# Kernel tuning notes

Measured on AMD Instinct MI355X. Metric: run time of the kernel, lower is better.

Reference implementation:

```python
import jax, jax.numpy as jnp
import numpy as np

N, T, D, H = 256, 128, 512, 1024


def setup_inputs() -> dict:
    key = jax.random.key(0)
    k_x, k_A, k_Wx, k_Wh, k_Wa = jax.random.split(key, 5)
    x = jax.random.normal(k_x, (N, T, D), dtype=jnp.float32)
    A = jax.random.normal(k_A, (N, H, 4, 4), dtype=jnp.float32)
    Wx = jax.random.normal(k_Wx, (D, 4 * H), dtype=jnp.float32) / np.sqrt(D)
    Wh = jax.random.normal(k_Wh, (H, 4 * H), dtype=jnp.float32) / np.sqrt(H)
    Wattn = jax.random.normal(k_Wa, (H, 4 * H), dtype=jnp.float32) / np.sqrt(H)
    b = jnp.zeros((4 * H,), dtype=jnp.float32)
    return {"x": x, "A": A, "Wx": Wx, "Wh": Wh, "Wattn": Wattn, "b": b}


def _attention_lstm(x, A, Wx, Wh, Wattn, b):
    # A: (N, H, 4, 4) -> flatten spatial to (N, H, 16)
    A_flat = A.reshape(A.shape[0], A.shape[1], -1)
    h0 = A_flat.mean(axis=2)  # (N, H)
    c0 = h0
    Hdim = h0.shape[1]
    scale = 1.0 / jnp.sqrt(jnp.asarray(Hdim, dtype=x.dtype))

    def step(carry, x_t):
        prev_h, prev_c = carry
        # scaled dot-product attention over 16 spatial locations
        scores = jnp.einsum("nh,nhs->ns", prev_h, A_flat) * scale  # (N, 16)
        w = jax.nn.softmax(scores, axis=1)
        attn = jnp.einsum("nhs,ns->nh", A_flat, w)  # (N, H)
        # fused LSTM gates
        a = x_t @ Wx + prev_h @ Wh + attn @ Wattn + b  # (N, 4H)
        i = jax.nn.sigmoid(a[:, 0:Hdim])
        f = jax.nn.sigmoid(a[:, Hdim:2 * Hdim])
        o = jax.nn.sigmoid(a[:, 2 * Hdim:3 * Hdim])
        g = jnp.tanh(a[:, 3 * Hdim:4 * Hdim])
        next_c = f * prev_c + i * g
        next_h = o * jnp.tanh(next_c)
        return (next_h, next_c), next_h

    x_tnd = jnp.swapaxes(x, 0, 1)  # (T, N, D)
    _, h_tnh = jax.lax.scan(step, (h0, c0), x_tnd)
    return jnp.swapaxes(h_tnh, 0, 1)  # (N, T, H)


def reference(x, A, Wx, Wh, Wattn, b):
    return _attention_lstm(x, A, Wx, Wh, Wattn, b)
```

## Files before the change

### kernel.cpp

```cpp
#include <hip/hip_runtime.h>
#include <math.h>

#define NB 256
#define TT 128
#define DD 512
#define HH 1024
#define KHX 1536
#define KFB 2560
#define BK 128
#define NBLK3 256
#define NCH3 16

typedef _Float16 half_t;
typedef _Float16 half8 __attribute__((ext_vector_type(8)));
typedef _Float16 half4v __attribute__((ext_vector_type(4)));
typedef _Float16 half2v __attribute__((ext_vector_type(2)));
typedef float f32x4 __attribute__((ext_vector_type(4)));


__global__ __launch_bounds__(256) void k_trans(const float* __restrict__ src,
        half_t* __restrict__ dst, int kstride, int koff, int nkt) {
    __shared__ half_t tile[64][65];
    int bk = blockIdx.x % nkt;
    int bn = blockIdx.x / nkt;
    int k0 = bk * 64, n0 = bn * 64;
    #pragma unroll
    for (int i = 0; i < 16; ++i) {
        int idx = i * 256 + threadIdx.x;
        int r = idx >> 6, c = idx & 63;
        tile[c][r] = (half_t)src[(size_t)(k0 + r) * 4096 + n0 + c];
    }
    __syncthreads();
    #pragma unroll
    for (int i = 0; i < 16; ++i) {
        int idx = i * 256 + threadIdx.x;
        int r = idx >> 6, c = idx & 63;
        dst[(size_t)(n0 + r) * kstride + koff + k0 + c] = tile[r][c];
    }
}

__global__ __launch_bounds__(256) void k_convX(const float* __restrict__ x,
        half_t* __restrict__ x16) {
    size_t base = ((size_t)blockIdx.x * 256 + threadIdx.x) * 32;
    #pragma unroll
    for (int u = 0; u < 4; ++u) {
        float4 a = ((const float4*)(x + base))[2 * u];
        float4 c = ((const float4*)(x + base))[2 * u + 1];
        half8 p;
        p[0] = (half_t)a.x; p[1] = (half_t)a.y; p[2] = (half_t)a.z; p[3] = (half_t)a.w;
        p[4] = (half_t)c.x; p[5] = (half_t)c.y; p[6] = (half_t)c.z; p[7] = (half_t)c.w;
        ((half8*)(x16 + base))[u] = p;
    }
}

__global__ __launch_bounds__(256) void k_convA(const float* __restrict__ A,
        half_t* __restrict__ A16, half_t* __restrict__ AsT,
        float* __restrict__ cbuf, half_t* __restrict__ h16,
        float* __restrict__ sc0, float* __restrict__ sc1, float* __restrict__ sc2) {
    __shared__ float sred[4][16];
    int n = blockIdx.x, tid = threadIdx.x;
    float ps[16];
    #pragma unroll
    for (int s = 0; s < 16; ++s) ps[s] = 0.f;
    #pragma unroll
    for (int r = 0; r < 4; ++r) {
        int h = tid + r * 256;
        const float4* ap = (const float4*)(A + ((size_t)n * HH + h) * 16);
        float4 v0 = ap[0], v1 = ap[1], v2 = ap[2], v3 = ap[3];
        float a[16];
        a[0]=v0.x; a[1]=v0.y; a[2] =v0.z; a[3] =v0.w;
        a[4]=v1.x; a[5]=v1.y; a[6] =v1.z; a[7] =v1.w;
        a[8]=v2.x; a[9]=v2.y; a[10]=v2.z; a[11]=v2.w;
        a[12]=v3.x; a[13]=v3.y; a[14]=v3.z; a[15]=v3.w;
        float hv = 0.f;
        #pragma unroll
        for (int s = 0; s < 16; ++s) hv += a[s];
        hv *= (1.f / 16.f);
        size_t ci = (size_t)n * HH + h;
        cbuf[ci] = hv;
        h16[ci] = (half_t)hv;
        half8 q0, q1;
        #pragma unroll
        for (int s = 0; s < 8; ++s) { q0[s] = (half_t)a[s]; q1[s] = (half_t)a[s + 8]; }
        *(half8*)(A16 + ci * 16) = q0;
        *(half8*)(A16 + ci * 16 + 8) = q1;
        #pragma unroll
        for (int s = 0; s < 16; ++s)
            AsT[(size_t)n * 16 * HH + (size_t)s * HH + h] = (half_t)a[s];
        #pragma unroll
        for (int s = 0; s < 16; ++s) ps[s] += hv * a[s];
    }
    #pragma unroll
    for (int off = 32; off; off >>= 1)
        #pragma unroll
        for (int s = 0; s < 16; ++s) ps[s] += __shfl_xor(ps[s], off, 64);
    int wave = tid >> 6;
    if ((tid & 63) == 0)
        #pragma unroll
        for (int s = 0; s < 16; ++s) sred[wave][s] = ps[s];
    __syncthreads();
    if (tid < 16) {
        sc0[n * 16 + tid] = sred[0][tid] + sred[1][tid] + sred[2][tid] + sred[3][tid];
        sc1[n * 16 + tid] = 0.f;
        sc2[n * 16 + tid] = 0.f;
    }
}

__global__ __launch_bounds__(256) void k_gemm_G(const half_t* __restrict__ AsT,
        const half_t* __restrict__ WaT, half_t* __restrict__ G16) {
    __shared__ half_t sAs[16][BK + 8];
    __shared__ half_t sB[4][16][BK + 8];
    int bid = blockIdx.x;
    int n = bid >> 6, jt = bid & 63;
    int j0 = jt * 16;
    int tid = threadIdx.x, wv = tid >> 6, lane = tid & 63;
    f32x4 acc = {};
    int srB = tid >> 2, scB = (tid & 3) * 32;
    int gB = srB >> 4, jcB = srB & 15;
    for (int it = 0; it < HH / BK; ++it) {
        int k0 = it * BK;
        if (tid < 128) {
            int r = tid >> 3, c = (tid & 7) * 16;
            const uint4* sp = (const uint4*)(AsT + (size_t)n * 16 * HH + (size_t)r * HH + k0 + c);
            uint4 u0 = sp[0], u1 = sp[1];
            *(uint4*)&sAs[r][c] = u0;
            *(uint4*)&sAs[r][c + 8] = u1;
        }
        {
            const half_t* src = WaT + ((size_t)(gB * HH + j0 + jcB)) * HH + k0 + scB;
            uint4 u0 = ((const uint4*)src)[0];
            uint4 u1 = ((const uint4*)src)[1];
            uint4 u2 = ((const uint4*)src)[2];
            uint4 u3 = ((const uint4*)src)[3];
            *((uint4*)&sB[gB][jcB][scB])      = u0;
            *((uint4*)&sB[gB][jcB][scB + 8])  = u1;
            *((uint4*)&sB[gB][jcB][scB + 16]) = u2;
            *((uint4*)&sB[gB][jcB][scB + 24]) = u3;
        }
        __syncthreads();
        int row16 = lane & 15, kg = lane >> 4;
        #pragma unroll
        for (int kc = 0; kc < BK / 32; ++kc) {
            half8 bf = *(const half8*)&sB[wv][row16][kc * 32 + kg * 8];
            half8 af = *(const half8*)&sAs[row16][kc * 32 + kg * 8];
            acc = __builtin_amdgcn_mfma_f32_16x16x32_f16(af, bf, acc, 0, 0, 0);
        }
        __syncthreads();
    }
    int col = lane & 15, rbase = (lane >> 4) * 4;
    size_t jf = (size_t)wv * HH + j0 + col;
    half4v o;
    o[0] = (half_t)acc[0]; o[1] = (half_t)acc[1];
    o[2] = (half_t)acc[2]; o[3] = (half_t)acc[3];
    *(half4v*)(G16 + ((size_t)n * 4096 + jf) * 16 + rbase) = o;
}

__global__ __launch_bounds__(256) void k_gemm_XW(const half_t* __restrict__ x16,
        const half_t* __restrict__ WhxT, half_t* __restrict__ XW16) {
    __shared__ half_t sA[128][72];
    __shared__ half_t sB[64][72];
    int bid = blockIdx.x;
    int bm = bid & 255;
    int bj = bid >> 8;
    int row0 = bm * 128;
    int col0 = bj * 64;
    int tid = threadIdx.x, wv = tid >> 6, lane = tid & 63;
    int la = lane & 15, kg = lane >> 4;
    int mh = wv & 1, jh = wv >> 1;
    f32x4 acc[4][2] = {};
    int srA = tid >> 1, scA = (tid & 1) * 32;
    int srB = tid >> 2, scB = (tid & 3) * 16;
    for (int c = 0; c < 8; ++c) {
        {
            const uint4* sp = (const uint4*)(x16 + (size_t)(row0 + srA) * DD + c * 64 + scA);
            uint4 u0 = sp[0], u1 = sp[1];
            *(uint4*)&sA[srA][scA] = u0;
            *(uint4*)&sA[srA][scA + 8] = u1;
        }
        {
            const uint4* sp = (const uint4*)(WhxT + (size_t)(col0 + srB) * KHX + c * 64 + scB);
            *(uint4*)&sB[srB][scB] = sp[0];
        }
        __syncthreads();
        #pragma unroll
        for (int ks = 0; ks < 2; ++ks) {
            half8 b0 = *(const half8*)&sB[jh * 32 + la][ks * 32 + kg * 8];
            half8 b1 = *(const half8*)&sB[jh * 32 + 16 + la][ks * 32 + kg * 8];
            #pragma unroll
            for (int m = 0; m < 4; ++m) {
                half8 af = *(const half8*)&sA[mh * 64 + m * 16 + la][ks * 32 + kg * 8];
                acc[m][0] = __builtin_amdgcn_mfma_f32_16x16x32_f16(af, b0, acc[m][0], 0, 0, 0);
                acc[m][1] = __builtin_amdgcn_mfma_f32_16x16x32_f16(af, b1, acc[m][1], 0, 0, 0);
            }
        }
        __syncthreads();
    }
    #pragma unroll
    for (int m = 0; m < 4; ++m)
        #pragma unroll
        for (int jt = 0; jt < 2; ++jt)
            #pragma unroll
            for (int q = 0; q < 4; ++q) {
                int R = row0 + mh * 64 + m * 16 + kg * 4 + q;
                int C = col0 + jh * 32 + jt * 16 + la;
                int n = R >> 7, t = R & 127;
                int g = C >> 10, jrem = C & 1023;
                int jb = jrem >> 3, jj = jrem & 7;
                int mhalf = n >> 7, n_l = n & 127;
                size_t dst = ((((size_t)t * 128 + jb) * 2 + mhalf) * 128 + n_l) * 32
                           + g * 8 + jj;
                XW16[dst] = (half_t)acc[m][jt][q];
            }
}


struct StepLds3 {
    half_t W[32][1032];
    union {
        half_t H[2][128][72];
        struct {
            float pe[128][33];
            char  _pad[18432 - 16896];
            float ps[2][128][18];
        } e;
    } u;
};

__device__ __forceinline__ void grid_sync3(int* cnt, volatile int* flag, int inst) {
    __syncthreads();
    if (threadIdx.x == 0) {
        __threadfence();
        int prev = __hip_atomic_fetch_add(cnt, 1, __ATOMIC_ACQ_REL,
                                          __HIP_MEMORY_SCOPE_AGENT);
        if (prev == NBLK3 * (inst + 1) - 1) {
            __hip_atomic_store((int*)flag, inst + 1, __ATOMIC_RELEASE,
                               __HIP_MEMORY_SCOPE_AGENT);
        } else {
            int guard = 0;
            while (__hip_atomic_load((int*)flag, __ATOMIC_RELAXED,
                                     __HIP_MEMORY_SCOPE_AGENT) < inst + 1) {
                __builtin_amdgcn_s_sleep(2);
                if (++guard > (1 << 24)) break;
            }
        }
        __threadfence();
    }
    __syncthreads();
}

__global__ __launch_bounds__(512, 2) void k_steps3(
        const half_t* __restrict__ XW16, half_t* __restrict__ h16A,
        half_t* __restrict__ h16B, const half_t* __restrict__ WhxT,
        const half_t* __restrict__ A16, const half_t* __restrict__ G16,
        const float* __restrict__ b, const float* __restrict__ cbuf,
        float* __restrict__ sc0, float* __restrict__ sc1, float* __restrict__ sc2,
        float* __restrict__ out, int* __restrict__ bar) {
    __shared__ StepLds3 L;
    int bid = blockIdx.x;
    int mhalf = bid & 1, jb = bid >> 1;
    int n0 = mhalf * 128;
    int tid = threadIdx.x;
    int wv = tid >> 6, lane = tid & 63;
    int la = lane & 15, kg = lane >> 4;
    int kpar = wv & 1, sub = wv >> 1;
    int srow = tid >> 2, sseg = tid & 3;
    int* cnt = bar;
    volatile int* flag = (volatile int*)(bar + 32);

    {
        int wr = tid >> 4;
        int seg = tid & 15;
        const half_t* wsrc = WhxT + (size_t)((wr >> 3) * HH + jb * 8 + (wr & 7)) * KHX
                           + DD + seg * 64;
        #pragma unroll
        for (int i = 0; i < 8; ++i) {
            uint4 u = ((const uint4*)wsrc)[i];
            *(uint4*)&L.W[wr][seg * 64 + i * 8] = u;
        }
    }

    int n_l = tid & 127, jg2 = tid >> 7;
    int n = n0 + n_l;
    int jbase = jb * 8 + jg2 * 2;
    half8 gq[4][4];
    #pragma unroll
    for (int g = 0; g < 4; ++g) {
        const half8* gsrc = (const half8*)(G16 + ((size_t)n * 4096 + g * HH + jbase) * 16);
        #pragma unroll
        for (int i = 0; i < 4; ++i) gq[g][i] = gsrc[i];
    }
    half8 aq[4];
    {
        const half8* asrc = (const half8*)(A16 + ((size_t)n * HH + jbase) * 16);
        #pragma unroll
        for (int i = 0; i < 4; ++i) aq[i] = asrc[i];
    }
    float bb[4][2];
    #pragma unroll
    for (int g = 0; g < 4; ++g) {
        bb[g][0] = b[g * HH + jbase];
        bb[g][1] = b[g * HH + jbase + 1];
    }
    float creg[2];
    creg[0] = cbuf[(size_t)n * HH + jbase];
    creg[1] = cbuf[(size_t)n * HH + jbase + 1];

    float* scC = sc0; float* scN = sc1; float* scZ = sc2;
    half_t* h16c = h16A;
    half_t* h16n = h16B;

    uint4 rA0, rA1, rB0, rB1;

#define LOADC_A(c) { const uint4* sp_ = (const uint4*)(h16c + \
        (size_t)(n0 + srow) * HH + (c) * 64 + sseg * 16); \
        rA0 = sp_[0]; rA1 = sp_[1]; }
#define LOADC_B(c) { const uint4* sp_ = (const uint4*)(h16c + \
        (size_t)(n0 + srow) * HH + (c) * 64 + sseg * 16); \
        rB0 = sp_[0]; rB1 = sp_[1]; }
#define WRITE_A(BUF) { *(uint4*)&L.u.H[BUF][srow][sseg * 16] = rA0; \
                       *(uint4*)&L.u.H[BUF][srow][sseg * 16 + 8] = rA1; }
#define WRITE_B(BUF) { *(uint4*)&L.u.H[BUF][srow][sseg * 16] = rB0; \
                       *(uint4*)&L.u.H[BUF][srow][sseg * 16 + 8] = rB1; }
#define COMPUTE(BUF, c) { \
    _Pragma("unroll") \
    for (int ks = 0; ks < 2; ++ks) { \
        half8 a0 = *(const half8*)&L.u.H[BUF][sub * 32 + la][ks * 32 + kg * 8]; \
        half8 a1 = *(const half8*)&L.u.H[BUF][sub * 32 + 16 + la][ks * 32 + kg * 8]; \
        half8 b0 = *(const half8*)&L.W[la][(c) * 64 + ks * 32 + kg * 8]; \
        half8 b1 = *(const half8*)&L.W[16 + la][(c) * 64 + ks * 32 + kg * 8]; \
        acc00 = __builtin_amdgcn_mfma_f32_16x16x32_f16(a0, b0, acc00, 0, 0, 0); \
        acc01 = __builtin_amdgcn_mfma_f32_16x16x32_f16(a0, b1, acc01, 0, 0, 0); \
        acc10 = __builtin_amdgcn_mfma_f32_16x16x32_f16(a1, b0, acc10, 0, 0, 0); \
        acc11 = __builtin_amdgcn_mfma_f32_16x16x32_f16(a1, b1, acc11, 0, 0, 0); \
    } }

    for (int t = 0; t < TT; ++t) {
        const half_t* xwp = XW16 + ((((size_t)t * 128 + jb) * 2 + mhalf) * 128 + n_l) * 32;
        half2v xw2[4];
        #pragma unroll
        for (int g = 0; g < 4; ++g) xw2[g] = *(const half2v*)(xwp + g * 8 + (jg2 & 0) + 0 + (jbase - jb * 8 - jg2 * 2) + jg2 * 2);
        float w16[16];
        {
            const float4* sp = (const float4*)(scC + (size_t)n * 16);
            float4 q0 = sp[0], q1 = sp[1], q2 = sp[2], q3 = sp[3];
            float sc[16] = {q0.x, q0.y, q0.z, q0.w, q1.x, q1.y, q1.z, q1.w,
                            q2.x, q2.y, q2.z, q2.w, q3.x, q3.y, q3.z, q3.w};
            float m = -1e30f;
            #pragma unroll
            for (int s = 0; s < 16; ++s) { sc[s] *= 0.03125f; m = fmaxf(m, sc[s]); }
            float den = 0.f;
            #pragma unroll
            for (int s = 0; s < 16; ++s) { sc[s] = expf(sc[s] - m); den += sc[s]; }
            float inv = 1.f / den;
            #pragma unroll
            for (int s = 0; s < 16; ++s) w16[s] = sc[s] * inv;
        }
        if (bid < 8) scZ[bid * 512 + tid] = 0.f;

        f32x4 acc00 = {}, acc01 = {}, acc10 = {}, acc11 = {};
        LOADC_A(0); WRITE_A(0); LOADC_B(1);
        __syncthreads();
        #pragma unroll 1
        for (int d = 0; d < 8; ++d) {
            int c0 = 2 * d, c1 = 2 * d + 1;
            if (kpar == 0) COMPUTE(0, c0);
            WRITE_B(1);
            if (c0 + 2 < NCH3) LOADC_A(c0 + 2);
            __syncthreads();
            if (kpar == 1) COMPUTE(1, c1);
            if (c0 + 2 < NCH3) WRITE_A(0);
            if (c1 + 2 < NCH3) LOADC_B(c1 + 2);
            __syncthreads();
        }

        if (kpar == 0) {
            #pragma unroll
            for (int q = 0; q < 4; ++q) {
                L.u.e.pe[sub * 32 + kg * 4 + q][la]           = acc00[q];
                L.u.e.pe[sub * 32 + kg * 4 + q][16 + la]      = acc01[q];
                L.u.e.pe[sub * 32 + 16 + kg * 4 + q][la]      = acc10[q];
                L.u.e.pe[sub * 32 + 16 + kg * 4 + q][16 + la] = acc11[q];
            }
        }
        __syncthreads();
        if (kpar == 1) {
            #pragma unroll
            for (int q = 0; q < 4; ++q) {
                L.u.e.pe[sub * 32 + kg * 4 + q][la]           += acc00[q];
                L.u.e.pe[sub * 32 + kg * 4 + q][16 + la]      += acc01[q];
                L.u.e.pe[sub * 32 + 16 + kg * 4 + q][la]      += acc10[q];
                L.u.e.pe[sub * 32 + 16 + kg * 4 + q][16 + la] += acc11[q];
            }
        }
        __syncthreads();

        float v[4][2];
        #pragma unroll
        for (int g = 0; g < 4; ++g) {
            #pragma unroll
            for (int jj = 0; jj < 2; ++jj) {
                float a0 = 0.f;
                #pragma unroll
                for (int s = 0; s < 16; ++s)
                    a0 += w16[s] * (float)gq[g][jj * 2 + (s >> 3)][s & 7];
                v[g][jj] = L.u.e.pe[n_l][g * 8 + jg2 * 2 + jj] + bb[g][jj]
                         + (float)xw2[g][jj] + a0;
            }
        }
        float hv[2];
        #pragma unroll
        for (int jj = 0; jj < 2; ++jj) {
            float ig = 1.f / (1.f + expf(-v[0][jj]));
            float fg = 1.f / (1.f + expf(-v[1][jj]));
            float og = 1.f / (1.f + expf(-v[2][jj]));
            float gg = tanhf(v[3][jj]);
            float cn = fg * creg[jj] + ig * gg;
            creg[jj] = cn;
            hv[jj] = og * tanhf(cn);
        }
        {
            float2 o2; o2.x = hv[0]; o2.y = hv[1];
            *(float2*)(out + ((size_t)n * TT + t) * HH + jbase) = o2;
            half2v h2; h2[0] = (half_t)hv[0]; h2[1] = (half_t)hv[1];
            *(half2v*)(h16n + (size_t)n * HH + jbase) = h2;
        }
        float p[16];
        #pragma unroll
        for (int s = 0; s < 16; ++s)
            p[s] = hv[0] * (float)aq[s >> 3][s & 7]
                 + hv[1] * (float)aq[2 + (s >> 3)][s & 7];
        int pair = jg2 >> 1;
        if ((jg2 & 1) == 0) {
            #pragma unroll
            for (int s = 0; s < 16; ++s) L.u.e.ps[pair][n_l][s] = p[s];
        }
        __syncthreads();
        if ((jg2 & 1) == 1) {
            #pragma unroll
            for (int s = 0; s < 16; ++s) L.u.e.ps[pair][n_l][s] += p[s];
        }
        __syncthreads();
        {
            #pragma unroll
            for (int i = 0; i < 4; ++i) {
                int slot = tid * 4 + i;
                int nn = slot >> 4, s = slot & 15;
                float val = L.u.e.ps[0][nn][s] + L.u.e.ps[1][nn][s];
                atomicAdd(scN + (size_t)(n0 + nn) * 16 + s, val);
            }
        }

        if (t + 1 < TT) grid_sync3(cnt, flag, t);
        float* tmp = scC; scC = scN; scN = scZ; scZ = tmp;
        half_t* th = h16c; h16c = h16n; h16n = th;
    }
#undef LOADC_A
#undef LOADC_B
#undef WRITE_A
#undef WRITE_B
#undef COMPUTE
}


union LdsS {
    struct {
        half_t sA[32][BK + 8];
        half_t sB[4][16][BK + 8];
    } s;
    float pe[4][32][16];
};

__global__ __launch_bounds__(256) void k_step(const float* __restrict__ x,
        const half_t* __restrict__ h16c, half_t* __restrict__ h16n,
        const half_t* __restrict__ WhxT, const half_t* __restrict__ A16,
        const half_t* __restrict__ G16, const float* __restrict__ b,
        float* __restrict__ cbuf, const float* __restrict__ scC,
        float* __restrict__ scN, float* __restrict__ scZ,
        float* __restrict__ out, int t) {
    __shared__ LdsS L;
    __shared__ float wlds[32][16];
    int bid = blockIdx.x;
    int xcd = bid & 7, slot = bid >> 3;
    int mtile = slot & 7, jtile = slot >> 3;
    int n0 = mtile * 32;
    int j0 = xcd * 128 + jtile * 16;
    int tid = threadIdx.x, wv = tid >> 6, lane = tid & 63;

    if (bid < 16) scZ[bid * 256 + tid] = 0.f;
    if (tid < 32) {
        int n = n0 + tid;
        const float4* sp = (const float4*)(scC + n * 16);
        float4 u0 = sp[0], u1 = sp[1], u2 = sp[2], u3 = sp[3];
        float sc[16] = {u0.x, u0.y, u0.z, u0.w, u1.x, u1.y, u1.z, u1.w,
                        u2.x, u2.y, u2.z, u2.w, u3.x, u3.y, u3.z, u3.w};
        float m = -1e30f;
        #pragma unroll
        for (int s = 0; s < 16; ++s) { sc[s] *= 0.03125f; m = fmaxf(m, sc[s]); }
        float den = 0.f;
        #pragma unroll
        for (int s = 0; s < 16; ++s) { sc[s] = expf(sc[s] - m); den += sc[s]; }
        float inv = 1.f / den;
        #pragma unroll
        for (int s = 0; s < 16; ++s) wlds[tid][s] = sc[s] * inv;
    }

    f32x4 acc[2] = {};
    int srA = tid >> 3, scA = (tid & 7) * 16;
    int srB = tid >> 2, scB = (tid & 3) * 32;
    int gB = srB >> 4, jcB = srB & 15;

    for (int it = 0; it < KHX / BK; ++it) {
        int k0 = it * BK;
        {
            int n = n0 + srA;
            if (k0 < DD) {
                const float* src = x + ((size_t)n * TT + t) * DD + k0 + scA;
                float4 v0 = ((const float4*)src)[0];
                float4 v1 = ((const float4*)src)[1];
                float4 v2 = ((const float4*)src)[2];
                float4 v3 = ((const float4*)src)[3];
                half8 p0, p1;
                p0[0] = (half_t)v0.x; p0[1] = (half_t)v0.y; p0[2] = (half_t)v0.z; p0[3] = (half_t)v0.w;
                p0[4] = (half_t)v1.x; p0[5] = (half_t)v1.y; p0[6] = (half_t)v1.z; p0[7] = (half_t)v1.w;
                p1[0] = (half_t)v2.x; p1[1] = (half_t)v2.y; p1[2] = (half_t)v2.z; p1[3] = (half_t)v2.w;
                p1[4] = (half_t)v3.x; p1[5] = (half_t)v3.y; p1[6] = (half_t)v3.z; p1[7] = (half_t)v3.w;
                *(half8*)&L.s.sA[srA][scA]     = p0;
                *(half8*)&L.s.sA[srA][scA + 8] = p1;
            } else {
                const half_t* srch = h16c + (size_t)n * HH + (k0 - DD) + scA;
                uint4 u0 = ((const uint4*)srch)[0];
                uint4 u1 = ((const uint4*)srch)[1];
                *((uint4*)&L.s.sA[srA][scA])     = u0;
                *((uint4*)&L.s.sA[srA][scA + 8]) = u1;
            }
        }
        {
            const half_t* src = WhxT + ((size_t)(gB * HH + j0 + jcB)) * KHX + k0 + scB;
            uint4 u0 = ((const uint4*)src)[0];
            uint4 u1 = ((const uint4*)src)[1];
            uint4 u2 = ((const uint4*)src)[2];
            uint4 u3 = ((const uint4*)src)[3];
            *((uint4*)&L.s.sB[gB][jcB][scB])      = u0;
            *((uint4*)&L.s.sB[gB][jcB][scB + 8])  = u1;
            *((uint4*)&L.s.sB[gB][jcB][scB + 16]) = u2;
            *((uint4*)&L.s.sB[gB][jcB][scB + 24]) = u3;
        }
        __syncthreads();
        int row16 = lane & 15, kg = lane >> 4;
        #pragma unroll
        for (int kc = 0; kc < BK / 32; ++kc) {
            half8 bf = *(const half8*)&L.s.sB[wv][row16][kc * 32 + kg * 8];
            #pragma unroll
            for (int m = 0; m < 2; ++m) {
                half8 af = *(const half8*)&L.s.sA[row16 + m * 16][kc * 32 + kg * 8];
                acc[m] = __builtin_amdgcn_mfma_f32_16x16x32_f16(af, bf, acc[m], 0, 0, 0);
            }
        }
        __syncthreads();
    }
    {
        int col = lane & 15, rbase = (lane >> 4) * 4;
        #pragma unroll
        for (int m = 0; m < 2; ++m)
            #pragma unroll
            for (int q = 0; q < 4; ++q)
                L.pe[wv][m * 16 + rbase + q][col] = acc[m][q];
    }
    __syncthreads();
    #pragma unroll
    for (int q2 = 0; q2 < 2; ++q2) {
        int idx = tid + q2 * 256;
        int r = idx >> 4, jc = idx & 15;
        int n = n0 + r, j = j0 + jc;
        float wv16[16];
        #pragma unroll
        for (int s = 0; s < 16; ++s) wv16[s] = wlds[r][s];
        float v[4];
        v[0] = L.pe[0][r][jc] + b[j];
        v[1] = L.pe[1][r][jc] + b[HH + j];
        v[2] = L.pe[2][r][jc] + b[2 * HH + j];
        v[3] = L.pe[3][r][jc] + b[3 * HH + j];
        #pragma unroll
        for (int g = 0; g < 4; ++g) {
            const half8* gq = (const half8*)(G16 + ((size_t)n * 4096 + g * HH + j) * 16);
            half8 ga = gq[0], gb2 = gq[1];
            float a0 = 0.f;
            #pragma unroll
            for (int s = 0; s < 8; ++s)
                a0 += wv16[s] * (float)ga[s] + wv16[s + 8] * (float)gb2[s];
            v[g] += a0;
        }
        float ig = 1.f / (1.f + expf(-v[0]));
        float fg = 1.f / (1.f + expf(-v[1]));
        float og = 1.f / (1.f + expf(-v[2]));
        float gg = tanhf(v[3]);
        size_t ci = (size_t)n * HH + j;
        float cp = cbuf[ci];
        float cn = fg * cp + ig * gg;
        cbuf[ci] = cn;
        float hv = og * tanhf(cn);
        out[((size_t)n * TT + t) * HH + j] = hv;
        h16n[ci] = (half_t)hv;
        const half8* ap = (const half8*)(A16 + ci * 16);
        half8 a0 = ap[0], a1 = ap[1];
        float p[16];
        #pragma unroll
        for (int s = 0; s < 8; ++s) { p[s] = hv * (float)a0[s]; p[s + 8] = hv * (float)a1[s]; }
        #pragma unroll
        for (int msk = 1; msk < 16; msk <<= 1)
            #pragma unroll
            for (int s = 0; s < 16; ++s) p[s] += __shfl_xor(p[s], msk, 64);
        float myp = 0.f;
        #pragma unroll
        for (int s = 0; s < 16; ++s) myp = (jc == s) ? p[s] : myp;
        atomicAdd(scN + n * 16 + jc, myp);
    }
}


__global__ __launch_bounds__(256) void fb_wconv(const float* __restrict__ Wx,
        const float* __restrict__ Wh, const float* __restrict__ Wa,
        half_t* __restrict__ WT) {
    __shared__ half_t tile[64][65];
    int bk = blockIdx.x % 40;
    int bn = blockIdx.x / 40;
    int k0 = bk * 64, n0 = bn * 64;
    #pragma unroll
    for (int i = 0; i < 16; ++i) {
        int idx = i * 256 + threadIdx.x;
        int r = idx >> 6, c = idx & 63;
        int k = k0 + r, n = n0 + c;
        float v;
        if (k < DD)            v = Wx[(size_t)k * 4096 + n];
        else if (k < DD + HH)  v = Wh[(size_t)(k - DD) * 4096 + n];
        else                   v = Wa[(size_t)(k - DD - HH) * 4096 + n];
        tile[c][r] = (half_t)v;
    }
    __syncthreads();
    #pragma unroll
    for (int i = 0; i < 16; ++i) {
        int idx = i * 256 + threadIdx.x;
        int r = idx >> 6, c = idx & 63;
        WT[(size_t)(n0 + r) * KFB + k0 + c] = tile[r][c];
    }
}

__global__ __launch_bounds__(256) void fb_init(const float* __restrict__ A,
        float* __restrict__ h0, float* __restrict__ c0) {
    int n = blockIdx.x;
    #pragma unroll
    for (int r = 0; r < 4; ++r) {
        int h = threadIdx.x + r * 256;
        const float4* ap = (const float4*)(A + ((size_t)n * HH + h) * 16);
        float s = 0.f;
        #pragma unroll
        for (int q = 0; q < 4; ++q) {
            float4 v = ap[q];
            s += v.x + v.y + v.z + v.w;
        }
        s *= (1.f / 16.f);
        h0[n * HH + h] = s;
        c0[n * HH + h] = s;
    }
}

__global__ __launch_bounds__(256) void fb_attn(const float* __restrict__ A,
        const float* __restrict__ hprev, long long hstride,
        half_t* __restrict__ h16, half_t* __restrict__ attn16) {
    __shared__ float sh[HH];
    __shared__ float sred[4][16];
    int n = blockIdx.x;
    const float* hp = hprev + (size_t)n * hstride;
    #pragma unroll
    for (int r = 0; r < 4; ++r) {
        int h = threadIdx.x + r * 256;
        float v = hp[h];
        sh[h] = v;
        h16[n * HH + h] = (half_t)v;
    }
    __syncthreads();
    float a[4][16];
    float ps[16];
    #pragma unroll
    for (int s = 0; s < 16; ++s) ps[s] = 0.f;
    #pragma unroll
    for (int r = 0; r < 4; ++r) {
        int h = threadIdx.x + r * 256;
        const float4* ap = (const float4*)(A + ((size_t)n * HH + h) * 16);
        float4 v0 = ap[0], v1 = ap[1], v2 = ap[2], v3 = ap[3];
        a[r][0] = v0.x;  a[r][1] = v0.y;  a[r][2]  = v0.z;  a[r][3]  = v0.w;
        a[r][4] = v1.x;  a[r][5] = v1.y;  a[r][6]  = v1.z;  a[r][7]  = v1.w;
        a[r][8] = v2.x;  a[r][9] = v2.y;  a[r][10] = v2.z;  a[r][11] = v2.w;
        a[r][12] = v3.x; a[r][13] = v3.y; a[r][14] = v3.z;  a[r][15] = v3.w;
        float hh = sh[h];
        #pragma unroll
        for (int s = 0; s < 16; ++s) ps[s] += hh * a[r][s];
    }
    #pragma unroll
    for (int off = 32; off; off >>= 1)
        #pragma unroll
        for (int s = 0; s < 16; ++s) ps[s] += __shfl_xor(ps[s], off, 64);
    int wave = threadIdx.x >> 6;
    if ((threadIdx.x & 63) == 0)
        #pragma unroll
        for (int s = 0; s < 16; ++s) sred[wave][s] = ps[s];
    __syncthreads();
    float sc[16], m = -1e30f;
    #pragma unroll
    for (int s = 0; s < 16; ++s) {
        sc[s] = (sred[0][s] + sred[1][s] + sred[2][s] + sred[3][s]) * 0.03125f;
        m = fmaxf(m, sc[s]);
    }
    float den = 0.f;
    #pragma unroll
    for (int s = 0; s < 16; ++s) { sc[s] = expf(sc[s] - m); den += sc[s]; }
    float inv = 1.f / den;
    #pragma unroll
    for (int r = 0; r < 4; ++r) {
        int h = threadIdx.x + r * 256;
        float acc = 0.f;
        #pragma unroll
        for (int s = 0; s < 16; ++s) acc += a[r][s] * sc[s];
        attn16[n * HH + h] = (half_t)(acc * inv);
    }
}

union LdsFB {
    struct {
        half_t sA[32][BK + 8];
        half_t sB[4][16][BK + 8];
    } s;
    float pe[4][32][16];
};

__global__ __launch_bounds__(256) void fb_gemm(const float* __restrict__ x,
        const half_t* __restrict__ h16, const half_t* __restrict__ attn16,
        const half_t* __restrict__ WT, const float* __restrict__ b,
        float* __restrict__ cbuf, float* __restrict__ out, int t) {
    __shared__ LdsFB L;
    int bid = blockIdx.x;
    int xcd = bid & 7;
    int slot = bid >> 3;
    int mtile = slot & 7;
    int jtile = slot >> 3;
    int m0 = mtile * 32;
    int j0 = xcd * 128 + jtile * 16;
    int tid = threadIdx.x;
    int wv = tid >> 6, lane = tid & 63;
    f32x4 acc[2] = {};
    int srA = tid >> 3, scA = (tid & 7) * 16;
    int srB = tid >> 2, scB = (tid & 3) * 32;
    int gB = srB >> 4, jcB = srB & 15;
    for (int it = 0; it < KFB / BK; ++it) {
        int k0 = it * BK;
        {
            int n = m0 + srA;
            if (k0 < DD) {
                const float* src = x + ((size_t)n * TT + t) * DD + k0 + scA;
                float4 v0 = ((const float4*)src)[0];
                float4 v1 = ((const float4*)src)[1];
                float4 v2 = ((const float4*)src)[2];
                float4 v3 = ((const float4*)src)[3];
                half8 p0, p1;
                p0[0] = (half_t)v0.x; p0[1] = (half_t)v0.y; p0[2] = (half_t)v0.z; p0[3] = (half_t)v0.w;
                p0[4] = (half_t)v1.x; p0[5] = (half_t)v1.y; p0[6] = (half_t)v1.z; p0[7] = (half_t)v1.w;
                p1[0] = (half_t)v2.x; p1[1] = (half_t)v2.y; p1[2] = (half_t)v2.z; p1[3] = (half_t)v2.w;
                p1[4] = (half_t)v3.x; p1[5] = (half_t)v3.y; p1[6] = (half_t)v3.z; p1[7] = (half_t)v3.w;
                *(half8*)&L.s.sA[srA][scA]     = p0;
                *(half8*)&L.s.sA[srA][scA + 8] = p1;
            } else {
                const half_t* srch = (k0 < DD + HH)
                    ? (h16    + (size_t)n * HH + (k0 - DD)      + scA)
                    : (attn16 + (size_t)n * HH + (k0 - DD - HH) + scA);
                uint4 u0 = ((const uint4*)srch)[0];
                uint4 u1 = ((const uint4*)srch)[1];
                *((uint4*)&L.s.sA[srA][scA])     = u0;
                *((uint4*)&L.s.sA[srA][scA + 8]) = u1;
            }
        }
        {
            const half_t* src = WT + ((size_t)(gB * HH + j0 + jcB)) * KFB + k0 + scB;
            uint4 u0 = ((const uint4*)src)[0];
            uint4 u1 = ((const uint4*)src)[1];
            uint4 u2 = ((const uint4*)src)[2];
            uint4 u3 = ((const uint4*)src)[3];
            *((uint4*)&L.s.sB[gB][jcB][scB])      = u0;
            *((uint4*)&L.s.sB[gB][jcB][scB + 8])  = u1;
            *((uint4*)&L.s.sB[gB][jcB][scB + 16]) = u2;
            *((uint4*)&L.s.sB[gB][jcB][scB + 24]) = u3;
        }
        __syncthreads();
        int row16 = lane & 15, kg = lane >> 4;
        #pragma unroll
        for (int kc = 0; kc < BK / 32; ++kc) {
            half8 bf = *(const half8*)&L.s.sB[wv][row16][kc * 32 + kg * 8];
            #pragma unroll
            for (int m = 0; m < 2; ++m) {
                half8 af = *(const half8*)&L.s.sA[row16 + m * 16][kc * 32 + kg * 8];
                acc[m] = __builtin_amdgcn_mfma_f32_16x16x32_f16(af, bf, acc[m], 0, 0, 0);
            }
        }
        __syncthreads();
    }
    {
        int col = lane & 15, rbase = (lane >> 4) * 4;
        #pragma unroll
        for (int m = 0; m < 2; ++m)
            #pragma unroll
            for (int q = 0; q < 4; ++q)
                L.pe[wv][m * 16 + rbase + q][col] = acc[m][q];
    }
    __syncthreads();
    #pragma unroll
    for (int q2 = 0; q2 < 2; ++q2) {
        int idx = tid + q2 * 256;
        int r = idx >> 4, jc = idx & 15;
        int n = m0 + r, j = j0 + jc;
        float vi = L.pe[0][r][jc] + b[j];
        float vf = L.pe[1][r][jc] + b[HH + j];
        float vo = L.pe[2][r][jc] + b[2 * HH + j];
        float vg = L.pe[3][r][jc] + b[3 * HH + j];
        float ig = 1.f / (1.f + expf(-vi));
        float fg = 1.f / (1.f + expf(-vf));
        float og = 1.f / (1.f + expf(-vo));
        float gg = tanhf(vg);
        size_t ci = (size_t)n * HH + j;
        float cp = cbuf[ci];
        float cn = fg * cp + ig * gg;
        cbuf[ci] = cn;
        out[((size_t)n * TT + t) * HH + j] = og * tanhf(cn);
    }
}


extern "C" void kernel_launch(void* const* d_in, const int* in_sizes, int n_in,
                              void* d_out, int out_size, void* d_ws, size_t ws_size,
                              hipStream_t stream) {
    const float* x  = (const float*)d_in[0];
    const float* A  = (const float*)d_in[1];
    const float* Wx = (const float*)d_in[2];
    const float* Wh = (const float*)d_in[3];
    const float* Wa = (const float*)d_in[4];
    const float* b  = (const float*)d_in[5];
    float* out = (float*)d_out;
    char* ws = (char*)d_ws;

    int maxb = 0;
    hipError_t oe = hipOccupancyMaxActiveBlocksPerMultiprocessor(&maxb, k_steps3, 512, 0);
    bool persistent_ok = (oe == hipSuccess && maxb >= 1);

    if (ws_size >= 375439616ULL && persistent_ok) {
        half_t* WhxT = (half_t*)(ws);
        half_t* WaT  = (half_t*)(ws + 12582912);
        half_t* A16  = (half_t*)(ws + 20971520);
        half_t* AsT  = (half_t*)(ws + 29360128);
        half_t* G16  = (half_t*)(ws + 37748736);
        half_t* h16a = (half_t*)(ws + 71303168);
        half_t* h16b = (half_t*)(ws + 71827456);
        float*  cb   = (float*) (ws + 72351744);
        float*  sc0  = (float*) (ws + 73400320);
        float*  sc1  = (float*) (ws + 73416704);
        float*  sc2  = (float*) (ws + 73433088);
        half_t* x16  = (half_t*)(ws + 73449472);
        int*    bar  = (int*)   (ws + 107003904);
        half_t* XW16 = (half_t*)(ws + 107004160);

        hipLaunchKernelGGL(k_trans, dim3(8 * 64),  dim3(256), 0, stream, Wx, WhxT, KHX, 0,   8);
        hipLaunchKernelGGL(k_trans, dim3(16 * 64), dim3(256), 0, stream, Wh, WhxT, KHX, 512, 16);
        hipLaunchKernelGGL(k_trans, dim3(16 * 64), dim3(256), 0, stream, Wa, WaT,  HH,  0,   16);
        hipLaunchKernelGGL(k_convX, dim3(2048), dim3(256), 0, stream, x, x16);
        hipLaunchKernelGGL(k_convA, dim3(256), dim3(256), 0, stream,
                           A, A16, AsT, cb, h16a, sc0, sc1, sc2);
        hipLaunchKernelGGL(k_gemm_G, dim3(NB * 64), dim3(256), 0, stream, AsT, WaT, G16);
        hipLaunchKernelGGL(k_gemm_XW, dim3(256 * 64), dim3(256), 0, stream, x16, WhxT, XW16);
        hipMemsetAsync(bar, 0, 256, stream);
        hipLaunchKernelGGL(k_steps3, dim3(NBLK3), dim3(512), 0, stream,
                           XW16, h16a, h16b, WhxT, A16, G16, b, cb,
                           sc0, sc1, sc2, out, bar);
    } else if (ws_size >= 73449472ULL) {
        half_t* WhxT = (half_t*)(ws);
        half_t* WaT  = (half_t*)(ws + 12582912);
        half_t* A16  = (half_t*)(ws + 20971520);
        half_t* AsT  = (half_t*)(ws + 29360128);
        half_t* G16  = (half_t*)(ws + 37748736);
        half_t* h16a = (half_t*)(ws + 71303168);
        half_t* h16b = (half_t*)(ws + 71827456);
        float*  cb   = (float*) (ws + 72351744);
        float*  sc0  = (float*) (ws + 73400320);
        float*  sc1  = (float*) (ws + 73416704);
        float*  sc2  = (float*) (ws + 73433088);
        float* scb[3] = {sc0, sc1, sc2};

        hipLaunchKernelGGL(k_trans, dim3(8 * 64),  dim3(256), 0, stream, Wx, WhxT, KHX, 0,   8);
        hipLaunchKernelGGL(k_trans, dim3(16 * 64), dim3(256), 0, stream, Wh, WhxT, KHX, 512, 16);
        hipLaunchKernelGGL(k_trans, dim3(16 * 64), dim3(256), 0, stream, Wa, WaT,  HH,  0,   16);
        hipLaunchKernelGGL(k_convA, dim3(256), dim3(256), 0, stream,
                           A, A16, AsT, cb, h16a, sc0, sc1, sc2);
        hipLaunchKernelGGL(k_gemm_G, dim3(NB * 64), dim3(256), 0, stream, AsT, WaT, G16);
        for (int t = 0; t < TT; ++t) {
            float* scC = scb[t % 3];
            float* scN = scb[(t + 1) % 3];
            float* scZ = scb[(t + 2) % 3];
            half_t* h16c = (t & 1) ? h16b : h16a;
            half_t* h16n = (t & 1) ? h16a : h16b;
            hipLaunchKernelGGL(k_step, dim3(512), dim3(256), 0, stream,
                               x, h16c, h16n, WhxT, A16, G16, b, cb, scC, scN, scZ, out, t);
        }
    } else {
        half_t* WT  = (half_t*)ws;
        float*  h0  = (float*)(ws + 20971520);
        float*  cb  = (float*)(ws + 22020096);
        half_t* h16 = (half_t*)(ws + 23068672);
        half_t* a16 = (half_t*)(ws + 23592960);
        hipLaunchKernelGGL(fb_wconv, dim3(2560), dim3(256), 0, stream, Wx, Wh, Wa, WT);
        hipLaunchKernelGGL(fb_init, dim3(256), dim3(256), 0, stream, A, h0, cb);
        for (int t = 0; t < TT; ++t) {
            const float* hp = (t == 0) ? h0 : (out + (size_t)(t - 1) * HH);
            long long hstride = (t == 0) ? (long long)HH : (long long)TT * HH;
            hipLaunchKernelGGL(fb_attn, dim3(256), dim3(256), 0, stream, A, hp, hstride, h16, a16);
            hipLaunchKernelGGL(fb_gemm, dim3(512), dim3(256), 0, stream,
                               x, h16, a16, WT, b, cb, out, t);
        }
    }
}
```

Measured before the change: 4.632 ms.

## Spread score atomics over 8 slices and restructure persistent step kernel

```diff
diff --git a/kernel.cpp b/kernel.cpp
--- a/kernel.cpp
+++ b/kernel.cpp
@@ -8,8 +8,7 @@
 #define KHX 1536
 #define KFB 2560
 #define BK 128
-#define NBLK3 256
-#define NCH3 16
+#define NBLK4 256
 
 typedef _Float16 half_t;
 typedef _Float16 half8 __attribute__((ext_vector_type(8)));
@@ -53,15 +52,10 @@
     }
 }
 
-__global__ __launch_bounds__(256) void k_convA(const float* __restrict__ A,
+__global__ __launch_bounds__(256) void k_convA2(const float* __restrict__ A,
         half_t* __restrict__ A16, half_t* __restrict__ AsT,
-        float* __restrict__ cbuf, half_t* __restrict__ h16,
-        float* __restrict__ sc0, float* __restrict__ sc1, float* __restrict__ sc2) {
-    __shared__ float sred[4][16];
+        float* __restrict__ cbuf, half_t* __restrict__ h16) {
     int n = blockIdx.x, tid = threadIdx.x;
-    float ps[16];
-    #pragma unroll
-    for (int s = 0; s < 16; ++s) ps[s] = 0.f;
     #pragma unroll
     for (int r = 0; r < 4; ++r) {
         int h = tid + r * 256;
@@ -87,8 +81,29 @@
         #pragma unroll
         for (int s = 0; s < 16; ++s)
             AsT[(size_t)n * 16 * HH + (size_t)s * HH + h] = (half_t)a[s];
-        #pragma unroll
-        for (int s = 0; s < 16; ++s) ps[s] += hv * a[s];
+    }
+}
+
+__global__ __launch_bounds__(256) void k_initsc(const half_t* __restrict__ h16,
+        const half_t* __restrict__ A16,
+        float* __restrict__ sc0, float* __restrict__ sc1, float* __restrict__ sc2) {
+    __shared__ float sred[4][16];
+    int n = blockIdx.x, tid = threadIdx.x;
+    float ps[16];
+    #pragma unroll
+    for (int s = 0; s < 16; ++s) ps[s] = 0.f;
+    #pragma unroll
+    for (int r = 0; r < 4; ++r) {
+        int h = tid + r * 256;
+        size_t ci = (size_t)n * HH + h;
+        float hv = (float)h16[ci];
+        const half8* ap = (const half8*)(A16 + ci * 16);
+        half8 a0 = ap[0], a1 = ap[1];
+        #pragma unroll
+        for (int s = 0; s < 8; ++s) {
+            ps[s]     += hv * (float)a0[s];
+            ps[s + 8] += hv * (float)a1[s];
+        }
     }
     #pragma unroll
     for (int off = 32; off; off >>= 1)
@@ -99,10 +114,17 @@
         #pragma unroll
         for (int s = 0; s < 16; ++s) sred[wave][s] = ps[s];
     __syncthreads();
-    if (tid < 16) {
-        sc0[n * 16 + tid] = sred[0][tid] + sred[1][tid] + sred[2][tid] + sred[3][tid];
-        sc1[n * 16 + tid] = 0.f;
-        sc2[n * 16 + tid] = 0.f;
+    if (tid < 16)
+        sc0[(size_t)n * 16 + tid] =
+            sred[0][tid] + sred[1][tid] + sred[2][tid] + sred[3][tid];
+    if (tid < 112) {
+        int x = 1 + tid / 16, s = tid % 16;
+        sc0[((size_t)x * 256 + n) * 16 + s] = 0.f;
+    }
+    if (tid < 128) {
+        int x = tid / 16, s = tid % 16;
+        sc1[((size_t)x * 256 + n) * 16 + s] = 0.f;
+        sc2[((size_t)x * 256 + n) * 16 + s] = 0.f;
     }
 }
 
@@ -195,45 +217,55 @@
         }
         __syncthreads();
     }
+    __syncthreads();
+    half_t (*Cl)[72] = sA;
     #pragma unroll
     for (int m = 0; m < 4; ++m)
         #pragma unroll
         for (int jt = 0; jt < 2; ++jt)
             #pragma unroll
             for (int q = 0; q < 4; ++q) {
-                int R = row0 + mh * 64 + m * 16 + kg * 4 + q;
-                int C = col0 + jh * 32 + jt * 16 + la;
-                int n = R >> 7, t = R & 127;
-                int g = C >> 10, jrem = C & 1023;
-                int jb = jrem >> 3, jj = jrem & 7;
-                int mhalf = n >> 7, n_l = n & 127;
-                size_t dst = ((((size_t)t * 128 + jb) * 2 + mhalf) * 128 + n_l) * 32
-                           + g * 8 + jj;
-                XW16[dst] = (half_t)acc[m][jt][q];
-            }
-}
-
-
-struct StepLds3 {
-    half_t W[32][1032];
+                int rl = mh * 64 + m * 16 + kg * 4 + q;
+                int cl = jh * 32 + jt * 16 + la;
+                Cl[rl][cl] = (half_t)acc[m][jt][q];
+            }
+    __syncthreads();
+    int g = col0 >> 10;
+    #pragma unroll
+    for (int i = 0; i < 4; ++i) {
+        int idx = tid + i * 256;
+        int rl = idx >> 3, grp = idx & 7;
+        int R = row0 + rl;
+        int t = R & 127, nn = R >> 7;
+        int mh2 = nn >> 7, nl2 = nn & 127;
+        int jb2 = ((col0 & 1023) >> 3) + grp;
+        size_t dst = ((((size_t)t * 128 + jb2) * 2 + mh2) * 128 + nl2) * 32 + g * 8;
+        *(half8*)(XW16 + dst) = *(const half8*)&Cl[rl][grp * 8];
+    }
+}
+
+
+struct StepLds4 {
+    half_t W[32][1028];
     union {
-        half_t H[2][128][72];
+        half_t H[128][260];
+        float sm[4][128][16];
         struct {
             float pe[128][33];
-            char  _pad[18432 - 16896];
+            float pad[896];
             float ps[2][128][18];
         } e;
     } u;
 };
 
-__device__ __forceinline__ void grid_sync3(int* cnt, volatile int* flag, int inst) {
+__device__ __forceinline__ void grid_sync4(int* cnt, volatile int* flag, int inst) {
     __syncthreads();
     if (threadIdx.x == 0) {
         __threadfence();
-        int prev = __hip_atomic_fetch_add(cnt, 1, __ATOMIC_ACQ_REL,
+        int prev = __hip_atomic_fetch_add(cnt, 1, __ATOMIC_RELAXED,
                                           __HIP_MEMORY_SCOPE_AGENT);
-        if (prev == NBLK3 * (inst + 1) - 1) {
-            __hip_atomic_store((int*)flag, inst + 1, __ATOMIC_RELEASE,
+        if (prev == NBLK4 * (inst + 1) - 1) {
+            __hip_atomic_store((int*)flag, inst + 1, __ATOMIC_RELAXED,
                                __HIP_MEMORY_SCOPE_AGENT);
         } else {
             int guard = 0;
@@ -248,35 +280,32 @@
     __syncthreads();
 }
 
-__global__ __launch_bounds__(512, 2) void k_steps3(
+__global__ __launch_bounds__(512, 1) void k_steps4(
         const half_t* __restrict__ XW16, half_t* __restrict__ h16A,
         half_t* __restrict__ h16B, const half_t* __restrict__ WhxT,
         const half_t* __restrict__ A16, const half_t* __restrict__ G16,
         const float* __restrict__ b, const float* __restrict__ cbuf,
         float* __restrict__ sc0, float* __restrict__ sc1, float* __restrict__ sc2,
         float* __restrict__ out, int* __restrict__ bar) {
-    __shared__ StepLds3 L;
+    __shared__ StepLds4 L;
     int bid = blockIdx.x;
     int mhalf = bid & 1, jb = bid >> 1;
     int n0 = mhalf * 128;
     int tid = threadIdx.x;
     int wv = tid >> 6, lane = tid & 63;
     int la = lane & 15, kg = lane >> 4;
-    int kpar = wv & 1, sub = wv >> 1;
     int srow = tid >> 2, sseg = tid & 3;
+    int slice = bid & 7;
     int* cnt = bar;
     volatile int* flag = (volatile int*)(bar + 32);
 
     {
-        int wr = tid >> 4;
-        int seg = tid & 15;
+        int wr = tid >> 4, seg = tid & 15;
         const half_t* wsrc = WhxT + (size_t)((wr >> 3) * HH + jb * 8 + (wr & 7)) * KHX
                            + DD + seg * 64;
         #pragma unroll
-        for (int i = 0; i < 8; ++i) {
-            uint4 u = ((const uint4*)wsrc)[i];
-            *(uint4*)&L.W[wr][seg * 64 + i * 8] = u;
-        }
+        for (int i = 0; i < 8; ++i)
+            *(uint4*)&L.W[wr][seg * 64 + i * 8] = ((const uint4*)wsrc)[i];
     }
 
     int n_l = tid & 127, jg2 = tid >> 7;
@@ -309,42 +338,43 @@
     half_t* h16c = h16A;
     half_t* h16n = h16B;
 
-    uint4 rA0, rA1, rB0, rB1;
-
-#define LOADC_A(c) { const uint4* sp_ = (const uint4*)(h16c + \
-        (size_t)(n0 + srow) * HH + (c) * 64 + sseg * 16); \
-        rA0 = sp_[0]; rA1 = sp_[1]; }
-#define LOADC_B(c) { const uint4* sp_ = (const uint4*)(h16c + \
-        (size_t)(n0 + srow) * HH + (c) * 64 + sseg * 16); \
-        rB0 = sp_[0]; rB1 = sp_[1]; }
-#define WRITE_A(BUF) { *(uint4*)&L.u.H[BUF][srow][sseg * 16] = rA0; \
-                       *(uint4*)&L.u.H[BUF][srow][sseg * 16 + 8] = rA1; }
-#define WRITE_B(BUF) { *(uint4*)&L.u.H[BUF][srow][sseg * 16] = rB0; \
-                       *(uint4*)&L.u.H[BUF][srow][sseg * 16 + 8] = rB1; }
-#define COMPUTE(BUF, c) { \
-    _Pragma("unroll") \
-    for (int ks = 0; ks < 2; ++ks) { \
-        half8 a0 = *(const half8*)&L.u.H[BUF][sub * 32 + la][ks * 32 + kg * 8]; \
-        half8 a1 = *(const half8*)&L.u.H[BUF][sub * 32 + 16 + la][ks * 32 + kg * 8]; \
-        half8 b0 = *(const half8*)&L.W[la][(c) * 64 + ks * 32 + kg * 8]; \
-        half8 b1 = *(const half8*)&L.W[16 + la][(c) * 64 + ks * 32 + kg * 8]; \
-        acc00 = __builtin_amdgcn_mfma_f32_16x16x32_f16(a0, b0, acc00, 0, 0, 0); \
-        acc01 = __builtin_amdgcn_mfma_f32_16x16x32_f16(a0, b1, acc01, 0, 0, 0); \
-        acc10 = __builtin_amdgcn_mfma_f32_16x16x32_f16(a1, b0, acc10, 0, 0, 0); \
-        acc11 = __builtin_amdgcn_mfma_f32_16x16x32_f16(a1, b1, acc11, 0, 0, 0); \
-    } }
+    half2v xwv[4];
+    {
+        const half_t* xwp = XW16 + (((size_t)jb * 2 + mhalf) * 128 + n_l) * 32;
+        #pragma unroll
+        for (int g = 0; g < 4; ++g) xwv[g] = *(const half2v*)(xwp + g * 8 + jg2 * 2);
+    }
 
     for (int t = 0; t < TT; ++t) {
-        const half_t* xwp = XW16 + ((((size_t)t * 128 + jb) * 2 + mhalf) * 128 + n_l) * 32;
-        half2v xw2[4];
-        #pragma unroll
-        for (int g = 0; g < 4; ++g) xw2[g] = *(const half2v*)(xwp + g * 8 + (jg2 & 0) + 0 + (jbase - jb * 8 - jg2 * 2) + jg2 * 2);
+        if (bid < 64) ((float*)scZ)[bid * 512 + tid] = 0.f;
+
+        {
+            const float* p0 = scC + ((size_t)(jg2 * 2) * 256 + n) * 16;
+            const float* p1 = scC + ((size_t)(jg2 * 2 + 1) * 256 + n) * 16;
+            #pragma unroll
+            for (int i = 0; i < 4; ++i) {
+                float4 a = ((const float4*)p0)[i];
+                float4 c = ((const float4*)p1)[i];
+                float4 o;
+                o.x = a.x + c.x; o.y = a.y + c.y; o.z = a.z + c.z; o.w = a.w + c.w;
+                *(float4*)&L.u.sm[jg2][n_l][4 * i] = o;
+            }
+        }
+        __syncthreads();
         float w16[16];
         {
-            const float4* sp = (const float4*)(scC + (size_t)n * 16);
-            float4 q0 = sp[0], q1 = sp[1], q2 = sp[2], q3 = sp[3];
-            float sc[16] = {q0.x, q0.y, q0.z, q0.w, q1.x, q1.y, q1.z, q1.w,
-                            q2.x, q2.y, q2.z, q2.w, q3.x, q3.y, q3.z, q3.w};
+            float sc[16];
+            #pragma unroll
+            for (int i = 0; i < 4; ++i) {
+                float4 q0 = *(const float4*)&L.u.sm[0][n_l][4 * i];
+                float4 q1 = *(const float4*)&L.u.sm[1][n_l][4 * i];
+                float4 q2 = *(const float4*)&L.u.sm[2][n_l][4 * i];
+                float4 q3 = *(const float4*)&L.u.sm[3][n_l][4 * i];
+                sc[4 * i + 0] = q0.x + q1.x + q2.x + q3.x;
+                sc[4 * i + 1] = q0.y + q1.y + q2.y + q3.y;
+                sc[4 * i + 2] = q0.z + q1.z + q2.z + q3.z;
+                sc[4 * i + 3] = q0.w + q1.w + q2.w + q3.w;
+            }
             float m = -1e30f;
             #pragma unroll
             for (int s = 0; s < 16; ++s) { sc[s] *= 0.03125f; m = fmaxf(m, sc[s]); }
@@ -355,42 +385,41 @@
             #pragma unroll
             for (int s = 0; s < 16; ++s) w16[s] = sc[s] * inv;
         }
-        if (bid < 8) scZ[bid * 512 + tid] = 0.f;
-
-        f32x4 acc00 = {}, acc01 = {}, acc10 = {}, acc11 = {};
-        LOADC_A(0); WRITE_A(0); LOADC_B(1);
+
+        f32x4 acc0 = {}, acc1 = {};
+        uint4 r[8];
+        {
+            const half_t* src = h16c + (size_t)(n0 + srow) * HH + sseg * 64;
+            #pragma unroll
+            for (int i = 0; i < 8; ++i) r[i] = ((const uint4*)src)[i];
+        }
         __syncthreads();
         #pragma unroll 1
-        for (int d = 0; d < 8; ++d) {
-            int c0 = 2 * d, c1 = 2 * d + 1;
-            if (kpar == 0) COMPUTE(0, c0);
-            WRITE_B(1);
-            if (c0 + 2 < NCH3) LOADC_A(c0 + 2);
+        for (int c = 0; c < 4; ++c) {
+            #pragma unroll
+            for (int i = 0; i < 8; ++i)
+                *(uint4*)&L.u.H[srow][sseg * 64 + i * 8] = r[i];
             __syncthreads();
-            if (kpar == 1) COMPUTE(1, c1);
-            if (c0 + 2 < NCH3) WRITE_A(0);
-            if (c1 + 2 < NCH3) LOADC_B(c1 + 2);
+            if (c + 1 < 4) {
+                const half_t* src = h16c + (size_t)(n0 + srow) * HH + (c + 1) * 256 + sseg * 64;
+                #pragma unroll
+                for (int i = 0; i < 8; ++i) r[i] = ((const uint4*)src)[i];
+            }
+            #pragma unroll
+            for (int ks = 0; ks < 8; ++ks) {
+                half8 af = *(const half8*)&L.u.H[wv * 16 + la][ks * 32 + kg * 8];
+                half8 b0 = *(const half8*)&L.W[la][c * 256 + ks * 32 + kg * 8];
+                half8 b1 = *(const half8*)&L.W[16 + la][c * 256 + ks * 32 + kg * 8];
+                acc0 = __builtin_amdgcn_mfma_f32_16x16x32_f16(af, b0, acc0, 0, 0, 0);
+                acc1 = __builtin_amdgcn_mfma_f32_16x16x32_f16(af, b1, acc1, 0, 0, 0);
+            }
             __syncthreads();
         }
 
-        if (kpar == 0) {
-            #pragma unroll
-            for (int q = 0; q < 4; ++q) {
-                L.u.e.pe[sub * 32 + kg * 4 + q][la]           = acc00[q];
-                L.u.e.pe[sub * 32 + kg * 4 + q][16 + la]      = acc01[q];
-                L.u.e.pe[sub * 32 + 16 + kg * 4 + q][la]      = acc10[q];
-                L.u.e.pe[sub * 32 + 16 + kg * 4 + q][16 + la] = acc11[q];
-            }
-        }
-        __syncthreads();
-        if (kpar == 1) {
-            #pragma unroll
-            for (int q = 0; q < 4; ++q) {
-                L.u.e.pe[sub * 32 + kg * 4 + q][la]           += acc00[q];
-                L.u.e.pe[sub * 32 + kg * 4 + q][16 + la]      += acc01[q];
-                L.u.e.pe[sub * 32 + 16 + kg * 4 + q][la]      += acc10[q];
-                L.u.e.pe[sub * 32 + 16 + kg * 4 + q][16 + la] += acc11[q];
-            }
+        #pragma unroll
+        for (int q = 0; q < 4; ++q) {
+            L.u.e.pe[wv * 16 + kg * 4 + q][la]      = acc0[q];
+            L.u.e.pe[wv * 16 + kg * 4 + q][16 + la] = acc1[q];
         }
         __syncthreads();
 
@@ -404,7 +433,7 @@
                 for (int s = 0; s < 16; ++s)
                     a0 += w16[s] * (float)gq[g][jj * 2 + (s >> 3)][s & 7];
                 v[g][jj] = L.u.e.pe[n_l][g * 8 + jg2 * 2 + jj] + bb[g][jj]
-                         + (float)xw2[g][jj] + a0;
+                         + (float)xwv[g][jj] + a0;
             }
         }
         float hv[2];
@@ -440,27 +469,81 @@
             for (int s = 0; s < 16; ++s) L.u.e.ps[pair][n_l][s] += p[s];
         }
         __syncthreads();
-        {
-            #pragma unroll
-            for (int i = 0; i < 4; ++i) {
-                int slot = tid * 4 + i;
-                int nn = slot >> 4, s = slot & 15;
-                float val = L.u.e.ps[0][nn][s] + L.u.e.ps[1][nn][s];
-                atomicAdd(scN + (size_t)(n0 + nn) * 16 + s, val);
-            }
-        }
-
-        if (t + 1 < TT) grid_sync3(cnt, flag, t);
+        #pragma unroll
+        for (int i = 0; i < 4; ++i) {
+            int slot = tid * 4 + i;
+            int nn = slot >> 4, s = slot & 15;
+            atomicAdd(scN + ((size_t)slice * 256 + n0 + nn) * 16 + s,
+                      L.u.e.ps[0][nn][s] + L.u.e.ps[1][nn][s]);
+        }
+
+        if (t + 1 < TT) {
+            half2v xwn[4];
+            const half_t* xwp = XW16 + ((((size_t)(t + 1) * 128 + jb) * 2 + mhalf) * 128 + n_l) * 32;
+            #pragma unroll
+            for (int g = 0; g < 4; ++g) xwn[g] = *(const half2v*)(xwp + g * 8 + jg2 * 2);
+            grid_sync4(cnt, flag, t);
+            #pragma unroll
+            for (int g = 0; g < 4; ++g) xwv[g] = xwn[g];
+        }
         float* tmp = scC; scC = scN; scN = scZ; scZ = tmp;
         half_t* th = h16c; h16c = h16n; h16n = th;
     }
-#undef LOADC_A
-#undef LOADC_B
-#undef WRITE_A
-#undef WRITE_B
-#undef COMPUTE
-}
-
+}
+
+
+__global__ __launch_bounds__(256) void k_convA(const float* __restrict__ A,
+        half_t* __restrict__ A16, half_t* __restrict__ AsT,
+        float* __restrict__ cbuf, half_t* __restrict__ h16,
+        float* __restrict__ sc0, float* __restrict__ sc1, float* __restrict__ sc2) {
+    __shared__ float sred[4][16];
+    int n = blockIdx.x, tid = threadIdx.x;
+    float ps[16];
+    #pragma unroll
+    for (int s = 0; s < 16; ++s) ps[s] = 0.f;
+    #pragma unroll
+    for (int r = 0; r < 4; ++r) {
+        int h = tid + r * 256;
+        const float4* ap = (const float4*)(A + ((size_t)n * HH + h) * 16);
+        float4 v0 = ap[0], v1 = ap[1], v2 = ap[2], v3 = ap[3];
+        float a[16];
+        a[0]=v0.x; a[1]=v0.y; a[2] =v0.z; a[3] =v0.w;
+        a[4]=v1.x; a[5]=v1.y; a[6] =v1.z; a[7] =v1.w;
+        a[8]=v2.x; a[9]=v2.y; a[10]=v2.z; a[11]=v2.w;
+        a[12]=v3.x; a[13]=v3.y; a[14]=v3.z; a[15]=v3.w;
+        float hv = 0.f;
+        #pragma unroll
+        for (int s = 0; s < 16; ++s) hv += a[s];
+        hv *= (1.f / 16.f);
+        size_t ci = (size_t)n * HH + h;
+        cbuf[ci] = hv;
+        h16[ci] = (half_t)hv;
+        half8 q0, q1;
+        #pragma unroll
+        for (int s = 0; s < 8; ++s) { q0[s] = (half_t)a[s]; q1[s] = (half_t)a[s + 8]; }
+        *(half8*)(A16 + ci * 16) = q0;
+        *(half8*)(A16 + ci * 16 + 8) = q1;
+        #pragma unroll
+        for (int s = 0; s < 16; ++s)
+            AsT[(size_t)n * 16 * HH + (size_t)s * HH + h] = (half_t)a[s];
+        #pragma unroll
+        for (int s = 0; s < 16; ++s) ps[s] += hv * a[s];
+    }
+    #pragma unroll
+    for (int off = 32; off; off >>= 1)
+        #pragma unroll
+        for (int s = 0; s < 16; ++s) ps[s] += __shfl_xor(ps[s], off, 64);
+    int wave = tid >> 6;
+    if ((tid & 63) == 0)
+        #pragma unroll
+        for (int s = 0; s < 16; ++s) sred[wave][s] = ps[s];
+    __syncthreads();
+    if (tid < 16) {
+        sc0[n * 16 + tid] = sred[0][tid] + sred[1][tid] + sred[2][tid] + sred[3][tid];
+        sc1[n * 16 + tid] = 0.f;
+        sc2[n * 16 + tid] = 0.f;
+    }
+}
 
 union LdsS {
     struct {
@@ -846,7 +929,7 @@
     char* ws = (char*)d_ws;
 
     int maxb = 0;
-    hipError_t oe = hipOccupancyMaxActiveBlocksPerMultiprocessor(&maxb, k_steps3, 512, 0);
+    hipError_t oe = hipOccupancyMaxActiveBlocksPerMultiprocessor(&maxb, k_steps4, 512, 0);
     bool persistent_ok = (oe == hipSuccess && maxb >= 1);
 
     if (ws_size >= 375439616ULL && persistent_ok) {
@@ -858,23 +941,23 @@
         half_t* h16a = (half_t*)(ws + 71303168);
         half_t* h16b = (half_t*)(ws + 71827456);
         float*  cb   = (float*) (ws + 72351744);
-        float*  sc0  = (float*) (ws + 73400320);
-        float*  sc1  = (float*) (ws + 73416704);
-        float*  sc2  = (float*) (ws + 73433088);
         half_t* x16  = (half_t*)(ws + 73449472);
         int*    bar  = (int*)   (ws + 107003904);
         half_t* XW16 = (half_t*)(ws + 107004160);
+        float*  sc0  = (float*)(ws + 29360128);
+        float*  sc1  = (float*)(ws + 29360128 + 32768);
+        float*  sc2  = (float*)(ws + 29360128 + 65536);
 
         hipLaunchKernelGGL(k_trans, dim3(8 * 64),  dim3(256), 0, stream, Wx, WhxT, KHX, 0,   8);
         hipLaunchKernelGGL(k_trans, dim3(16 * 64), dim3(256), 0, stream, Wh, WhxT, KHX, 512, 16);
         hipLaunchKernelGGL(k_trans, dim3(16 * 64), dim3(256), 0, stream, Wa, WaT,  HH,  0,   16);
         hipLaunchKernelGGL(k_convX, dim3(2048), dim3(256), 0, stream, x, x16);
-        hipLaunchKernelGGL(k_convA, dim3(256), dim3(256), 0, stream,
-                           A, A16, AsT, cb, h16a, sc0, sc1, sc2);
+        hipLaunchKernelGGL(k_convA2, dim3(256), dim3(256), 0, stream, A, A16, AsT, cb, h16a);
         hipLaunchKernelGGL(k_gemm_G, dim3(NB * 64), dim3(256), 0, stream, AsT, WaT, G16);
         hipLaunchKernelGGL(k_gemm_XW, dim3(256 * 64), dim3(256), 0, stream, x16, WhxT, XW16);
+        hipLaunchKernelGGL(k_initsc, dim3(256), dim3(256), 0, stream, h16a, A16, sc0, sc1, sc2);
         hipMemsetAsync(bar, 0, 256, stream);
-        hipLaunchKernelGGL(k_steps3, dim3(NBLK3), dim3(512), 0, stream,
+        hipLaunchKernelGGL(k_steps4, dim3(NBLK4), dim3(512), 0, stream,
                            XW16, h16a, h16b, WhxT, A16, G16, b, cb,
                            sc0, sc1, sc2, out, bar);
     } else if (ws_size >= 73449472ULL) {
```

Result: no change. 4.641 ms (+0.2%).
